# Performance work log

Measured on AMD Instinct MI355X. Metric: run time of the kernel, lower is better.

Reference implementation:

```python
import jax, jax.numpy as jnp
import numpy as np

DIM = 2048
RANK = 16
NUM_EXPERTS = 8


def setup_inputs() -> dict:
    key = jax.random.key(0)
    ks = jax.random.split(key, 8)
    x = jax.random.normal(ks[0], (4, 2048, DIM), dtype=jnp.float32)
    # router gate: nn.Linear(dim, num_experts) -> weight [E, dim], bias [E]
    gate_w = jax.random.normal(ks[1], (NUM_EXPERTS, DIM), dtype=jnp.float32) * 0.02
    gate_b = jnp.zeros((NUM_EXPERTS,), dtype=jnp.float32)
    # base_ffn: nn.Linear(dim, dim) -> weight [dim, dim], bias [dim]
    base_w = jax.random.normal(ks[2], (DIM, DIM), dtype=jnp.float32) * 0.02
    base_b = jnp.zeros((DIM,), dtype=jnp.float32)
    # LoRA experts, stacked: A maps dim->rank, B maps rank->dim (stored input-major)
    lora_A = jax.random.normal(ks[3], (NUM_EXPERTS, DIM, RANK), dtype=jnp.float32) * 0.02
    lora_B = jax.random.normal(ks[4], (NUM_EXPERTS, RANK, DIM), dtype=jnp.float32) * 0.02
    return {"x": x, "gate_w": gate_w, "gate_b": gate_b,
            "base_w": base_w, "base_b": base_b,
            "lora_A": lora_A, "lora_B": lora_B}


def reference(x, gate_w, gate_b, base_w, base_b, lora_A, lora_B):
    B, S, D = x.shape
    flat = x.reshape(-1, D)  # [T, D]
    # base FFN: Linear + exact GELU (torch default)
    base_out = jax.nn.gelu(flat @ base_w.T + base_b, approximate=False)
    # router: softmax then top-1
    probs = jax.nn.softmax(flat @ gate_w.T + gate_b, axis=-1)  # [T, E]
    idx = jnp.argmax(probs, axis=-1)                            # [T] top-1 index
    w = jnp.take_along_axis(probs, idx[:, None], axis=-1)      # [T, 1] top-1 weight
    E = lora_A.shape[0]
    expert_out = jnp.zeros_like(flat)
    for e in range(E):  # fixed small expert loop; GEMMs are dense over all tokens
        h = jax.nn.gelu(flat @ lora_A[e], approximate=False)   # [T, rank]
        ye = h @ lora_B[e]                                      # [T, D]
        sel = (idx == e)[:, None]
        expert_out = expert_out + jnp.where(sel, ye * w, 0.0)
    out = (base_out + expert_out).reshape(B, S, D)
    return out, probs
```

## Files before the change

### kernel.cpp

```cpp
#include <hip/hip_runtime.h>
#include <hip/hip_bf16.h>
#include <math.h>


#define DIM   2048
#define RANK  16
#define NEXP  8
#define NTOK  8192
#define KLORA 128

typedef __hip_bfloat16 bf16;
typedef __attribute__((ext_vector_type(8))) short short8;
typedef __attribute__((ext_vector_type(4))) float float4v;

typedef const __attribute__((address_space(1))) void* gptr_t;
typedef __attribute__((address_space(3))) void*       sptr_t;

__device__ __forceinline__ void async_ld16(const bf16* g, bf16* l) {
    __builtin_amdgcn_global_load_lds((gptr_t)g, (sptr_t)l, 16, 0, 0);
}

__device__ __forceinline__ float gelu_fast(float x) {
    float t = 0.7978845608028654f * (x + 0.044715f * x * x * x);
    t = fminf(fmaxf(t, -10.0f), 10.0f);
    float e = __expf(2.0f * t);
    float th = (e - 1.0f) / (e + 1.0f);
    return 0.5f * x * (1.0f + th);
}

__device__ __forceinline__ short8 pack8(float4 v0, float4 v1) {
    union { bf16 h[8]; short8 v; } u;
    u.h[0] = __float2bfloat16(v0.x); u.h[1] = __float2bfloat16(v0.y);
    u.h[2] = __float2bfloat16(v0.z); u.h[3] = __float2bfloat16(v0.w);
    u.h[4] = __float2bfloat16(v1.x); u.h[5] = __float2bfloat16(v1.y);
    u.h[6] = __float2bfloat16(v1.z); u.h[7] = __float2bfloat16(v1.w);
    return u.v;
}

__global__ __launch_bounds__(256) void cvt_logits_kernel(
    const float* __restrict__ x, const float* __restrict__ gate_w,
    const float* __restrict__ gate_b, const float* __restrict__ base_w,
    const float* __restrict__ lora_B, const float* __restrict__ lora_A,
    bf16* __restrict__ Xb, bf16* __restrict__ Wb,
    bf16* __restrict__ Bt, bf16* __restrict__ Ab,
    float* __restrict__ probs, int* __restrict__ idx_out, float* __restrict__ w_out)
{
    __shared__ float buf[2560];
    const int b   = blockIdx.x;
    const int tid = threadIdx.x;

    if (b < 1024) {
        const int t0 = b * 8;
        float4 g0[NEXP], g1[NEXP];
        #pragma unroll
        for (int e = 0; e < NEXP; e++) {
            const float* wr = gate_w + (size_t)e * DIM + tid * 8;
            g0[e] = *(const float4*)wr;
            g1[e] = *(const float4*)(wr + 4);
        }
        const int wave = tid >> 6, lane = tid & 63;
        #pragma unroll
        for (int tt = 0; tt < 8; tt++) {
            const int t = t0 + tt;
            const float* xr = x + (size_t)t * DIM + tid * 8;
            float4 v0 = *(const float4*)xr;
            float4 v1 = *(const float4*)(xr + 4);
            *(short8*)(Xb + (size_t)t * DIM + tid * 8) = pack8(v0, v1);
            float a[NEXP];
            #pragma unroll
            for (int e = 0; e < NEXP; e++) {
                a[e] = v0.x * g0[e].x + v0.y * g0[e].y + v0.z * g0[e].z + v0.w * g0[e].w
                     + v1.x * g1[e].x + v1.y * g1[e].y + v1.z * g1[e].z + v1.w * g1[e].w;
                #pragma unroll
                for (int off = 32; off > 0; off >>= 1) a[e] += __shfl_down(a[e], off);
            }
            if (lane == 0) {
                #pragma unroll
                for (int e = 0; e < NEXP; e++) buf[tt * 32 + wave * NEXP + e] = a[e];
            }
        }
        __syncthreads();
        if (tid < 8) {
            const int t = t0 + tid;
            float l[NEXP]; float mx = -1e30f;
            #pragma unroll
            for (int e = 0; e < NEXP; e++) {
                l[e] = buf[tid * 32 + e] + buf[tid * 32 + 8 + e]
                     + buf[tid * 32 + 16 + e] + buf[tid * 32 + 24 + e] + gate_b[e];
                mx = fmaxf(mx, l[e]);
            }
            float sum = 0.f;
            #pragma unroll
            for (int e = 0; e < NEXP; e++) { l[e] = __expf(l[e] - mx); sum += l[e]; }
            float inv = 1.0f / sum;
            int es = 0; float best = l[0];
            #pragma unroll
            for (int e = 1; e < NEXP; e++) if (l[e] > best) { best = l[e]; es = e; }
            #pragma unroll
            for (int e = 0; e < NEXP; e++) probs[(size_t)t * NEXP + e] = l[e] * inv;
            idx_out[t] = es;
            w_out[t]   = best * inv;
        }
    } else if (b < 1024 + 2048) {
        size_t v = ((size_t)(b - 1024) * 256 + tid) * 8;
        float4 v0 = *(const float4*)(base_w + v);
        float4 v1 = *(const float4*)(base_w + v + 4);
        *(short8*)(Wb + v) = pack8(v0, v1);
    } else if (b < 1024 + 2048 + 256) {
        int bb = b - 1024 - 2048;
        int kk0 = (bb >> 6) * 32, j0 = (bb & 63) * 32;
        {
            int r = tid >> 3, c4 = (tid & 7) * 4;
            float4 val = *(const float4*)(lora_B + (size_t)(kk0 + r) * DIM + j0 + c4);
            *(float4*)(buf + r * 36 + c4) = val;
        }
        __syncthreads();
        {
            int j = tid >> 3, k4 = (tid & 7) * 4;
            bf16* dst = Bt + (size_t)(j0 + j) * KLORA + kk0 + k4;
            #pragma unroll
            for (int i = 0; i < 4; i++) dst[i] = __float2bfloat16(buf[(k4 + i) * 36 + j]);
        }
    } else {
        int bb = b - 1024 - 2048 - 256;
        int e = bb >> 4, k0 = (bb & 15) * 128;
        const float* src = lora_A + (size_t)e * DIM * RANK;
        {
            int k = tid >> 2, r4 = (tid & 3) * 4;
            float4 va = *(const float4*)(src + (size_t)(k0 + k) * RANK + r4);
            float4 vb = *(const float4*)(src + (size_t)(k0 + k + 64) * RANK + r4);
            *(float4*)(buf + k * 20 + r4)        = va;
            *(float4*)(buf + (k + 64) * 20 + r4) = vb;
        }
        __syncthreads();
        {
            int r = tid >> 4, kx = (tid & 15) * 8;
            bf16* dst = Ab + (size_t)(e * 16 + r) * DIM + k0 + kx;
            #pragma unroll
            for (int i = 0; i < 8; i++) dst[i] = __float2bfloat16(buf[(kx + i) * 20 + r]);
        }
    }
}

__global__ __launch_bounds__(256) void hsel_kernel(
    const bf16* __restrict__ Xb, const bf16* __restrict__ Ab,
    const int* __restrict__ idx, const float* __restrict__ wsel,
    bf16* __restrict__ A2)
{
    __shared__ bf16 As[32 * 32];
    __shared__ bf16 Bs[64 * 32];
    const int tid  = threadIdx.x;
    const int wave = tid >> 6, lane = tid & 63;
    const int m0 = blockIdx.x * 32;
    const int n0 = blockIdx.y * 64;
    const int col = lane & 15, quad = lane >> 4;

    const int kc = ((tid & 3) ^ ((tid >> 3) & 3)) * 8;
    const bf16* gB = Ab + (size_t)(n0 + (tid >> 2)) * DIM + kc;
    const bf16* gA = Xb + (size_t)(m0 + (tid >> 2)) * DIM + kc;
    bf16* lB = Bs + wave * 512;
    bf16* lA = As + wave * 512;

    const int xr = quad ^ ((col >> 1) & 3);
    const bf16* pa = As + col * 32 + xr * 8;
    const bf16* pb = Bs + (wave * 16 + col) * 32 + xr * 8;

    float4v acc[2] = {};
    for (int k0 = 0; k0 < DIM; k0 += 32) {
        __syncthreads();
        async_ld16(gB + k0, lB);
        if (tid < 128) async_ld16(gA + k0, lA);
        __syncthreads();
        short8 a0 = *(const short8*)pa;
        short8 a1 = *(const short8*)(pa + 512);
        short8 b0 = *(const short8*)pb;
        acc[0] = __builtin_amdgcn_mfma_f32_16x16x32_bf16(a0, b0, acc[0], 0, 0, 0);
        acc[1] = __builtin_amdgcn_mfma_f32_16x16x32_bf16(a1, b0, acc[1], 0, 0, 0);
    }

    const int jcol = n0 + wave * 16 + col;
    const int ej   = jcol >> 4;
    #pragma unroll
    for (int i = 0; i < 2; i++) {
        int rbase = m0 + i * 16 + quad * 4;
        #pragma unroll
        for (int r = 0; r < 4; r++) {
            int t = rbase + r;
            float v = (idx[t] == ej) ? gelu_fast(acc[i][r]) * wsel[t] : 0.0f;
            A2[(size_t)t * KLORA + jcol] = __float2bfloat16(v);
        }
    }
}

__global__ __launch_bounds__(256, 3) void gemm_kernel(
    const bf16* __restrict__ Xb, const bf16* __restrict__ Wb,
    const float* __restrict__ base_b,
    const bf16* __restrict__ A2, const bf16* __restrict__ Bt,
    float* __restrict__ out)
{
    __shared__ bf16 As[128 * 64];
    __shared__ bf16 Bs[128 * 64];
    const int tid  = threadIdx.x;
    const int wave = tid >> 6, lane = tid & 63;
    const int wm = wave >> 1, wn = wave & 1;
    const int n0 = blockIdx.x * 128;
    const int m0 = blockIdx.y * 128;
    const int col = lane & 15, quad = lane >> 4;

    const int kc = (((tid & 7) ^ ((tid >> 3) & 7))) * 8;
    const int r0 = tid >> 3;
    const bf16* gA0 = Xb + (size_t)(m0 + r0) * DIM + kc;
    const bf16* gB0 = Wb + (size_t)(n0 + r0) * DIM + kc;
    const bf16* gA1 = gA0 + (size_t)32 * DIM;
    const bf16* gB1 = gB0 + (size_t)32 * DIM;
    const bf16* gA2 = gA0 + (size_t)64 * DIM;
    const bf16* gB2 = gB0 + (size_t)64 * DIM;
    const bf16* gA3 = gA0 + (size_t)96 * DIM;
    const bf16* gB3 = gB0 + (size_t)96 * DIM;
    bf16* lA = As + wave * 512;
    bf16* lB = Bs + wave * 512;

    const int sl0 = (quad        ^ (col & 7)) * 8;
    const int sl1 = ((quad | 4)  ^ (col & 7)) * 8;
    const bf16* paA = As + (wm * 64 + col) * 64;
    const bf16* pbB = Bs + (wn * 64 + col) * 64;

    float4v acc[4][4] = {};

    for (int k0 = 0; k0 < DIM; k0 += 64) {
        __syncthreads();
        async_ld16(gA0 + k0, lA);
        async_ld16(gA1 + k0, lA + 2048);
        async_ld16(gA2 + k0, lA + 4096);
        async_ld16(gA3 + k0, lA + 6144);
        async_ld16(gB0 + k0, lB);
        async_ld16(gB1 + k0, lB + 2048);
        async_ld16(gB2 + k0, lB + 4096);
        async_ld16(gB3 + k0, lB + 6144);
        __syncthreads();
        {
            short8 a[4], b[4];
            #pragma unroll
            for (int i = 0; i < 4; i++) a[i] = *(const short8*)(paA + i * 1024 + sl0);
            #pragma unroll
            for (int j = 0; j < 4; j++) b[j] = *(const short8*)(pbB + j * 1024 + sl0);
            #pragma unroll
            for (int i = 0; i < 4; i++)
                #pragma unroll
                for (int j = 0; j < 4; j++)
                    acc[i][j] = __builtin_amdgcn_mfma_f32_16x16x32_bf16(
                        a[i], b[j], acc[i][j], 0, 0, 0);
        }
        {
            short8 a[4], b[4];
            #pragma unroll
            for (int i = 0; i < 4; i++) a[i] = *(const short8*)(paA + i * 1024 + sl1);
            #pragma unroll
            for (int j = 0; j < 4; j++) b[j] = *(const short8*)(pbB + j * 1024 + sl1);
            #pragma unroll
            for (int i = 0; i < 4; i++)
                #pragma unroll
                for (int j = 0; j < 4; j++)
                    acc[i][j] = __builtin_amdgcn_mfma_f32_16x16x32_bf16(
                        a[i], b[j], acc[i][j], 0, 0, 0);
        }
    }

    float bias[4];
    #pragma unroll
    for (int j = 0; j < 4; j++) bias[j] = base_b[n0 + wn * 64 + j * 16 + col];
    #pragma unroll
    for (int i = 0; i < 4; i++)
        #pragma unroll
        for (int j = 0; j < 4; j++)
            #pragma unroll
            for (int r = 0; r < 4; r++)
                acc[i][j][r] = gelu_fast(acc[i][j][r] + bias[j]);

    const bf16* pea = A2 + (size_t)(m0 + wm * 64 + col) * KLORA + quad * 8;
    const bf16* peb = Bt + (size_t)(n0 + wn * 64 + col) * KLORA + quad * 8;
    #pragma unroll
    for (int ks = 0; ks < 4; ks++) {
        short8 ea[4], eb[4];
        #pragma unroll
        for (int i = 0; i < 4; i++)
            ea[i] = *(const short8*)(pea + i * 16 * KLORA + ks * 32);
        #pragma unroll
        for (int j = 0; j < 4; j++)
            eb[j] = *(const short8*)(peb + j * 16 * KLORA + ks * 32);
        #pragma unroll
        for (int i = 0; i < 4; i++)
            #pragma unroll
            for (int j = 0; j < 4; j++)
                acc[i][j] = __builtin_amdgcn_mfma_f32_16x16x32_bf16(
                    ea[i], eb[j], acc[i][j], 0, 0, 0);
    }

    #pragma unroll
    for (int i = 0; i < 4; i++) {
        #pragma unroll
        for (int j = 0; j < 4; j++) {
            int tt = m0 + wm * 64 + i * 16 + quad * 4;
            int jj = n0 + wn * 64 + j * 16 + col;
            float* po = out + (size_t)tt * DIM + jj;
            #pragma unroll
            for (int r = 0; r < 4; r++) po[(size_t)r * DIM] = acc[i][j][r];
        }
    }
}

extern "C" void kernel_launch(void* const* d_in, const int* in_sizes, int n_in,
                              void* d_out, int out_size, void* d_ws, size_t ws_size,
                              hipStream_t stream)
{
    (void)in_sizes; (void)n_in; (void)out_size; (void)ws_size;
    const float* x      = (const float*)d_in[0];
    const float* gate_w = (const float*)d_in[1];
    const float* gate_b = (const float*)d_in[2];
    const float* base_w = (const float*)d_in[3];
    const float* base_b = (const float*)d_in[4];
    const float* lora_A = (const float*)d_in[5];
    const float* lora_B = (const float*)d_in[6];

    float* out   = (float*)d_out;
    float* probs = out + (size_t)NTOK * DIM;

    char* ws = (char*)d_ws;
    bf16*  Xb   = (bf16*)ws;
    bf16*  Wb   = (bf16*)(ws + 33554432);
    bf16*  A2   = (bf16*)(ws + 41943040);
    bf16*  Bt   = (bf16*)(ws + 44040192);
    bf16*  Ab   = (bf16*)(ws + 44564480);
    int*   idx  = (int*) (ws + 45088768);
    float* wsel = (float*)(ws + 45121536);

    cvt_logits_kernel<<<1024 + 2048 + 256 + 128, 256, 0, stream>>>(
        x, gate_w, gate_b, base_w, lora_B, lora_A,
        Xb, Wb, Bt, Ab, probs, idx, wsel);
    hsel_kernel<<<dim3(256, 2), 256, 0, stream>>>(Xb, Ab, idx, wsel, A2);
    gemm_kernel<<<dim3(16, 64), 256, 0, stream>>>(Xb, Wb, base_b, A2, Bt, out);
}
```

Baseline: 253.2 us.

## Fuse router logits with LoRA down-projection and expert select, reorder GEMM grid

Router softmax/top-1 and the LoRA-A projection with GELU-and-select now run in one kernel, on 32-token blocks. Each block converts its x rows to bf16, computes logits, keeps the top-1 expert and weight in shared memory, then multiplies all 128 LoRA-A columns via MFMA. This removes the separate hsel launch and the global idx/weight round trip. The LoRA weight transposes move to a small prep kernel, and the main GEMM grid is transposed so blockIdx.x walks M. In exchange there are fewer router blocks with a serial 32-token loop, and the block depends on its own fresh global Xb writes being visible after a barrier.

```diff
diff --git a/kernel.cpp b/kernel.cpp
--- a/kernel.cpp
+++ b/kernel.cpp
@@ -37,20 +37,69 @@
     return u.v;
 }
 
-__global__ __launch_bounds__(256) void cvt_logits_kernel(
-    const float* __restrict__ x, const float* __restrict__ gate_w,
-    const float* __restrict__ gate_b, const float* __restrict__ base_w,
+__global__ __launch_bounds__(256) void prep_kernel(
     const float* __restrict__ lora_B, const float* __restrict__ lora_A,
-    bf16* __restrict__ Xb, bf16* __restrict__ Wb,
-    bf16* __restrict__ Bt, bf16* __restrict__ Ab,
-    float* __restrict__ probs, int* __restrict__ idx_out, float* __restrict__ w_out)
+    bf16* __restrict__ Bt, bf16* __restrict__ Ab)
 {
     __shared__ float buf[2560];
     const int b   = blockIdx.x;
     const int tid = threadIdx.x;
 
-    if (b < 1024) {
-        const int t0 = b * 8;
+    if (b < 256) {
+        int kk0 = (b >> 6) * 32, j0 = (b & 63) * 32;
+        {
+            int r = tid >> 3, c4 = (tid & 7) * 4;
+            float4 val = *(const float4*)(lora_B + (size_t)(kk0 + r) * DIM + j0 + c4);
+            *(float4*)(buf + r * 36 + c4) = val;
+        }
+        __syncthreads();
+        {
+            int j = tid >> 3, k4 = (tid & 7) * 4;
+            bf16* dst = Bt + (size_t)(j0 + j) * KLORA + kk0 + k4;
+            #pragma unroll
+            for (int i = 0; i < 4; i++) dst[i] = __float2bfloat16(buf[(k4 + i) * 36 + j]);
+        }
+    } else {
+        int bb = b - 256;
+        int e = bb >> 4, k0 = (bb & 15) * 128;
+        const float* src = lora_A + (size_t)e * DIM * RANK;
+        {
+            int k = tid >> 2, r4 = (tid & 3) * 4;
+            float4 va = *(const float4*)(src + (size_t)(k0 + k) * RANK + r4);
+            float4 vb = *(const float4*)(src + (size_t)(k0 + k + 64) * RANK + r4);
+            *(float4*)(buf + k * 20 + r4)        = va;
+            *(float4*)(buf + (k + 64) * 20 + r4) = vb;
+        }
+        __syncthreads();
+        {
+            int r = tid >> 4, kx = (tid & 15) * 8;
+            bf16* dst = Ab + (size_t)(e * 16 + r) * DIM + k0 + kx;
+            #pragma unroll
+            for (int i = 0; i < 8; i++) dst[i] = __float2bfloat16(buf[(kx + i) * 20 + r]);
+        }
+    }
+}
+
+__global__ __launch_bounds__(256, 4) void fused_kernel(
+    const float* __restrict__ x, const float* __restrict__ gate_w,
+    const float* __restrict__ gate_b, const float* __restrict__ base_w,
+    const bf16* __restrict__ Ab,
+    bf16* __restrict__ Xb, bf16* __restrict__ Wb, bf16* __restrict__ A2,
+    float* __restrict__ probs)
+{
+    const int b   = blockIdx.x;
+    const int tid = threadIdx.x;
+
+    if (b < 256) {
+        __shared__ bf16  Xs[32 * 64];
+        __shared__ bf16  Las[128 * 64];
+        __shared__ float lgbuf[32 * 32];
+        __shared__ float wtok[32];
+        __shared__ int   etok[32];
+
+        const int t0   = b * 32;
+        const int wave = tid >> 6, lane = tid & 63;
+
         float4 g0[NEXP], g1[NEXP];
         #pragma unroll
         for (int e = 0; e < NEXP; e++) {
@@ -58,9 +107,7 @@
             g0[e] = *(const float4*)wr;
             g1[e] = *(const float4*)(wr + 4);
         }
-        const int wave = tid >> 6, lane = tid & 63;
-        #pragma unroll
-        for (int tt = 0; tt < 8; tt++) {
+        for (int tt = 0; tt < 32; tt++) {
             const int t = t0 + tt;
             const float* xr = x + (size_t)t * DIM + tid * 8;
             float4 v0 = *(const float4*)xr;
@@ -76,17 +123,17 @@
             }
             if (lane == 0) {
                 #pragma unroll
-                for (int e = 0; e < NEXP; e++) buf[tt * 32 + wave * NEXP + e] = a[e];
-            }
-        }
-        __syncthreads();
-        if (tid < 8) {
+                for (int e = 0; e < NEXP; e++) lgbuf[tt * 32 + wave * NEXP + e] = a[e];
+            }
+        }
+        __syncthreads();
+        if (tid < 32) {
             const int t = t0 + tid;
             float l[NEXP]; float mx = -1e30f;
             #pragma unroll
             for (int e = 0; e < NEXP; e++) {
-                l[e] = buf[tid * 32 + e] + buf[tid * 32 + 8 + e]
-                     + buf[tid * 32 + 16 + e] + buf[tid * 32 + 24 + e] + gate_b[e];
+                l[e] = lgbuf[tid * 32 + e] + lgbuf[tid * 32 + 8 + e]
+                     + lgbuf[tid * 32 + 16 + e] + lgbuf[tid * 32 + 24 + e] + gate_b[e];
                 mx = fmaxf(mx, l[e]);
             }
             float sum = 0.f;
@@ -98,97 +145,65 @@
             for (int e = 1; e < NEXP; e++) if (l[e] > best) { best = l[e]; es = e; }
             #pragma unroll
             for (int e = 0; e < NEXP; e++) probs[(size_t)t * NEXP + e] = l[e] * inv;
-            idx_out[t] = es;
-            w_out[t]   = best * inv;
-        }
-    } else if (b < 1024 + 2048) {
-        size_t v = ((size_t)(b - 1024) * 256 + tid) * 8;
+            etok[tid] = es;
+            wtok[tid] = best * inv;
+        }
+
+        const int col = lane & 15, quad = lane >> 4;
+        const int kc  = ((tid & 7) ^ ((tid >> 3) & 7)) * 8;
+        const int row = tid >> 3;
+        const bf16* gX = Xb + (size_t)(t0 + row) * DIM + kc;
+        const bf16* gL = Ab + (size_t)row * DIM + kc;
+        bf16* lX = Xs  + wave * 512;
+        bf16* lL = Las + wave * 512;
+
+        const int sl0 = (quad       ^ (col & 7)) * 8;
+        const int sl1 = ((quad | 4) ^ (col & 7)) * 8;
+        const bf16* pa = Xs  + col * 64;
+        const bf16* pb = Las + (wave * 32 + col) * 64;
+
+        float4v acc[2][2] = {};
+        for (int k0 = 0; k0 < DIM; k0 += 64) {
+            __syncthreads();
+            async_ld16(gX + k0, lX);
+            async_ld16(gL + k0,                        lL);
+            async_ld16(gL + (size_t)32 * DIM + k0,     lL + 2048);
+            async_ld16(gL + (size_t)64 * DIM + k0,     lL + 4096);
+            async_ld16(gL + (size_t)96 * DIM + k0,     lL + 6144);
+            __syncthreads();
+            #pragma unroll
+            for (int ks = 0; ks < 2; ks++) {
+                const int sl = ks ? sl1 : sl0;
+                short8 a0 = *(const short8*)(pa + sl);
+                short8 a1 = *(const short8*)(pa + 1024 + sl);
+                short8 b0 = *(const short8*)(pb + sl);
+                short8 b1 = *(const short8*)(pb + 1024 + sl);
+                acc[0][0] = __builtin_amdgcn_mfma_f32_16x16x32_bf16(a0, b0, acc[0][0], 0, 0, 0);
+                acc[0][1] = __builtin_amdgcn_mfma_f32_16x16x32_bf16(a0, b1, acc[0][1], 0, 0, 0);
+                acc[1][0] = __builtin_amdgcn_mfma_f32_16x16x32_bf16(a1, b0, acc[1][0], 0, 0, 0);
+                acc[1][1] = __builtin_amdgcn_mfma_f32_16x16x32_bf16(a1, b1, acc[1][1], 0, 0, 0);
+            }
+        }
+
+        #pragma unroll
+        for (int i = 0; i < 2; i++) {
+            #pragma unroll
+            for (int jt = 0; jt < 2; jt++) {
+                const int jcol = wave * 32 + jt * 16 + col;
+                const int ej   = jcol >> 4;
+                #pragma unroll
+                for (int r = 0; r < 4; r++) {
+                    const int tl = i * 16 + quad * 4 + r;
+                    float v = (etok[tl] == ej) ? gelu_fast(acc[i][jt][r]) * wtok[tl] : 0.0f;
+                    A2[(size_t)(t0 + tl) * KLORA + jcol] = __float2bfloat16(v);
+                }
+            }
+        }
+    } else {
+        size_t v = ((size_t)(b - 256) * 256 + tid) * 8;
         float4 v0 = *(const float4*)(base_w + v);
         float4 v1 = *(const float4*)(base_w + v + 4);
         *(short8*)(Wb + v) = pack8(v0, v1);
-    } else if (b < 1024 + 2048 + 256) {
-        int bb = b - 1024 - 2048;
-        int kk0 = (bb >> 6) * 32, j0 = (bb & 63) * 32;
-        {
-            int r = tid >> 3, c4 = (tid & 7) * 4;
-            float4 val = *(const float4*)(lora_B + (size_t)(kk0 + r) * DIM + j0 + c4);
-            *(float4*)(buf + r * 36 + c4) = val;
-        }
-        __syncthreads();
-        {
-            int j = tid >> 3, k4 = (tid & 7) * 4;
-            bf16* dst = Bt + (size_t)(j0 + j) * KLORA + kk0 + k4;
-            #pragma unroll
-            for (int i = 0; i < 4; i++) dst[i] = __float2bfloat16(buf[(k4 + i) * 36 + j]);
-        }
-    } else {
-        int bb = b - 1024 - 2048 - 256;
-        int e = bb >> 4, k0 = (bb & 15) * 128;
-        const float* src = lora_A + (size_t)e * DIM * RANK;
-        {
-            int k = tid >> 2, r4 = (tid & 3) * 4;
-            float4 va = *(const float4*)(src + (size_t)(k0 + k) * RANK + r4);
-            float4 vb = *(const float4*)(src + (size_t)(k0 + k + 64) * RANK + r4);
-            *(float4*)(buf + k * 20 + r4)        = va;
-            *(float4*)(buf + (k + 64) * 20 + r4) = vb;
-        }
-        __syncthreads();
-        {
-            int r = tid >> 4, kx = (tid & 15) * 8;
-            bf16* dst = Ab + (size_t)(e * 16 + r) * DIM + k0 + kx;
-            #pragma unroll
-            for (int i = 0; i < 8; i++) dst[i] = __float2bfloat16(buf[(kx + i) * 20 + r]);
-        }
-    }
-}
-
-__global__ __launch_bounds__(256) void hsel_kernel(
-    const bf16* __restrict__ Xb, const bf16* __restrict__ Ab,
-    const int* __restrict__ idx, const float* __restrict__ wsel,
-    bf16* __restrict__ A2)
-{
-    __shared__ bf16 As[32 * 32];
-    __shared__ bf16 Bs[64 * 32];
-    const int tid  = threadIdx.x;
-    const int wave = tid >> 6, lane = tid & 63;
-    const int m0 = blockIdx.x * 32;
-    const int n0 = blockIdx.y * 64;
-    const int col = lane & 15, quad = lane >> 4;
-
-    const int kc = ((tid & 3) ^ ((tid >> 3) & 3)) * 8;
-    const bf16* gB = Ab + (size_t)(n0 + (tid >> 2)) * DIM + kc;
-    const bf16* gA = Xb + (size_t)(m0 + (tid >> 2)) * DIM + kc;
-    bf16* lB = Bs + wave * 512;
-    bf16* lA = As + wave * 512;
-
-    const int xr = quad ^ ((col >> 1) & 3);
-    const bf16* pa = As + col * 32 + xr * 8;
-    const bf16* pb = Bs + (wave * 16 + col) * 32 + xr * 8;
-
-    float4v acc[2] = {};
-    for (int k0 = 0; k0 < DIM; k0 += 32) {
-        __syncthreads();
-        async_ld16(gB + k0, lB);
-        if (tid < 128) async_ld16(gA + k0, lA);
-        __syncthreads();
-        short8 a0 = *(const short8*)pa;
-        short8 a1 = *(const short8*)(pa + 512);
-        short8 b0 = *(const short8*)pb;
-        acc[0] = __builtin_amdgcn_mfma_f32_16x16x32_bf16(a0, b0, acc[0], 0, 0, 0);
-        acc[1] = __builtin_amdgcn_mfma_f32_16x16x32_bf16(a1, b0, acc[1], 0, 0, 0);
-    }
-
-    const int jcol = n0 + wave * 16 + col;
-    const int ej   = jcol >> 4;
-    #pragma unroll
-    for (int i = 0; i < 2; i++) {
-        int rbase = m0 + i * 16 + quad * 4;
-        #pragma unroll
-        for (int r = 0; r < 4; r++) {
-            int t = rbase + r;
-            float v = (idx[t] == ej) ? gelu_fast(acc[i][r]) * wsel[t] : 0.0f;
-            A2[(size_t)t * KLORA + jcol] = __float2bfloat16(v);
-        }
     }
 }
 
@@ -203,8 +218,8 @@
     const int tid  = threadIdx.x;
     const int wave = tid >> 6, lane = tid & 63;
     const int wm = wave >> 1, wn = wave & 1;
-    const int n0 = blockIdx.x * 128;
-    const int m0 = blockIdx.y * 128;
+    const int m0 = blockIdx.x * 128;
+    const int n0 = blockIdx.y * 128;
     const int col = lane & 15, quad = lane >> 4;
 
     const int kc = (((tid & 7) ^ ((tid >> 3) & 7))) * 8;
@@ -331,12 +346,9 @@
     bf16*  A2   = (bf16*)(ws + 41943040);
     bf16*  Bt   = (bf16*)(ws + 44040192);
     bf16*  Ab   = (bf16*)(ws + 44564480);
-    int*   idx  = (int*) (ws + 45088768);
-    float* wsel = (float*)(ws + 45121536);
-
-    cvt_logits_kernel<<<1024 + 2048 + 256 + 128, 256, 0, stream>>>(
-        x, gate_w, gate_b, base_w, lora_B, lora_A,
-        Xb, Wb, Bt, Ab, probs, idx, wsel);
-    hsel_kernel<<<dim3(256, 2), 256, 0, stream>>>(Xb, Ab, idx, wsel, A2);
-    gemm_kernel<<<dim3(16, 64), 256, 0, stream>>>(Xb, Wb, base_b, A2, Bt, out);
-}
+
+    prep_kernel<<<384, 256, 0, stream>>>(lora_B, lora_A, Bt, Ab);
+    fused_kernel<<<256 + 2048, 256, 0, stream>>>(
+        x, gate_w, gate_b, base_w, Ab, Xb, Wb, A2, probs);
+    gemm_kernel<<<dim3(64, 16), 256, 0, stream>>>(Xb, Wb, base_b, A2, Bt, out);
+}
```

Measured after the change: 264.3 us. +4.4%, slower.
